# Kernel optimization log

Hardware: AMD Instinct MI355X
Metric: run time of the kernel (lower is better)

The kernel has to match this reference:

```python
import jax, jax.numpy as jnp
import numpy as np

N_STEPS = 8  # fixed-step RK4 over t in [0, 1]


def setup_inputs() -> dict:
    key = jax.random.key(0)
    ks = jax.random.split(key, 5)
    B, T, F, C = 64, 4096, 76, 15
    x = jax.random.normal(ks[0], (B, T, F), dtype=jnp.float32)
    # Conv1d(76->76, k=3) weights, PyTorch OIH layout, fan-in scaled
    conv_w = jax.random.normal(ks[1], (F, F, 3), dtype=jnp.float32) * (1.0 / np.sqrt(F * 3))
    conv_b = jax.random.normal(ks[2], (F,), dtype=jnp.float32) * 0.01
    final_w = jax.random.normal(ks[3], (C, F), dtype=jnp.float32) * (1.0 / np.sqrt(F))
    final_b = jax.random.normal(ks[4], (C,), dtype=jnp.float32) * 0.01
    return {"x": x, "conv_w": conv_w, "conv_b": conv_b,
            "final_w": final_w, "final_b": final_b}


def _func(h, conv_w, conv_b):
    # h: [B, F, T]; Conv1d k=3 pad=1 -> Tanh (the ODE vector field)
    y = jax.lax.conv_general_dilated(
        h, conv_w, window_strides=(1,), padding=[(1, 1)],
        dimension_numbers=("NCH", "OIH", "NCH"))
    return jnp.tanh(y + conv_b[None, :, None])


def reference(x, conv_w, conv_b, final_w, final_b):
    # x: [B, T, F] -> permute to channels-first for Conv1d
    h0 = jnp.transpose(x, (0, 2, 1))  # [B, F, T]
    dt = jnp.float32(1.0 / N_STEPS)

    def rk4_step(h, _):
        k1 = _func(h, conv_w, conv_b)
        k2 = _func(h + 0.5 * dt * k1, conv_w, conv_b)
        k3 = _func(h + 0.5 * dt * k2, conv_w, conv_b)
        k4 = _func(h + dt * k3, conv_w, conv_b)
        return h + (dt / 6.0) * (k1 + 2.0 * k2 + 2.0 * k3 + k4), None

    hT, _ = jax.lax.scan(rk4_step, h0, None, length=N_STEPS)
    # back to [B, T, F], then final Linear(F -> num_classes)
    out = jnp.einsum("bft,cf->btc", hT, final_w) + final_b
    return out
```

## Files before the change

kernel.cpp:

```cpp
#include <hip/hip_runtime.h>
#include <cstdint>
#include <cstddef>

#define F_CH 76
#define T_LEN 4096
#define B_TOT 64
#define C_CLS 15
#define NSTEP 8

#define W_OUT  144
#define HALO2  8
#define NBT    29
#define NKB    5
#define WSTR   88
#define SST    128
#define SROWS  162
#define TPB    960
#define HP     80

#define C2LOG2E 2.8853900817779268f

typedef __attribute__((ext_vector_type(8)))  __bf16 bf16x8;
typedef __attribute__((ext_vector_type(4)))  __bf16 bf16x4;
typedef __attribute__((ext_vector_type(16))) float  f32x16;
typedef __attribute__((ext_vector_type(4)))  float  f32x4;

__device__ __forceinline__ int sw_off(int r, int v) {
    return r * SST + (((v) ^ (r & 15)) << 3);
}

__global__ __launch_bounds__(256) void pad_copy_kernel(
    const float* __restrict__ x, __bf16* __restrict__ h, int b0)
{
    int bl = blockIdx.y;
    int q  = blockIdx.x * 256 + threadIdx.x;
    int t  = q / 20, c4 = (q - t * 20) * 4;
    float4 v = {0.f, 0.f, 0.f, 0.f};
    if (c4 < F_CH)
        v = *(const float4*)(x + ((size_t)(b0 + bl) * T_LEN + t) * F_CH + c4);
    bf16x4 p;
    p[0] = (__bf16)v.x; p[1] = (__bf16)v.y; p[2] = (__bf16)v.z; p[3] = (__bf16)v.w;
    *(bf16x4*)(h + ((size_t)bl * T_LEN + t) * HP + c4) = p;
}

__global__ __launch_bounds__(256) void wprep_kernel(
    const float* __restrict__ cw, __bf16* __restrict__ wpb)
{
    int idx = blockIdx.x * 256 + threadIdx.x;
    if (idx >= 3 * 96 * WSTR) return;
    int tap = idx / (96 * WSTR);
    int rem = idx - tap * 96 * WSTR;
    int c = rem / WSTR, ci = rem - c * WSTR;
    float v = 0.0f;
    if (c < F_CH && ci < F_CH) v = cw[((size_t)c * F_CH + ci) * 3 + tap];
    wpb[idx] = (__bf16)v;
}

__global__ __launch_bounds__(TPB, 4) void rk4_step2_kernel(
    const __bf16* __restrict__ hin, __bf16* __restrict__ hout,
    const __bf16* __restrict__ wpb, const float* __restrict__ cb)
{
    __shared__ __bf16 s_lds[2][SROWS * SST];
    __shared__ float  cb_lds[96];

    const int b    = blockIdx.y;
    const int T0   = blockIdx.x * W_OUT;
    const int tid  = threadIdx.x;
    const int lane = tid & 63;
    const int l31  = lane & 31;
    const int l5   = lane >> 5;
    const int wv   = tid >> 6;
    const int ct   = wv / 5;
    const int tq   = wv - ct * 5;

    const int  rb  = tq * 32 + l31;
    const int  tg  = T0 - HALO2 + rb;
    const bool tok = (tg >= 0 && tg < T_LEN);

    if (tid < 256) {
        int bi = tid / 128, rr = (tid % 128) / 64, c = tid % 64;
        ((uint32_t*)&s_lds[bi][(rr ? (SROWS - 1) : 0) * SST])[c] = 0u;
    }
    if (tid < 96) cb_lds[tid] = (tid < F_CH) ? cb[tid] * C2LOG2E : 0.0f;

    float  hn[16];
    bf16x4 hpk[4];
    const __bf16* hb = hin + (size_t)b * T_LEN * HP;
    #pragma unroll
    for (int q = 0; q < 4; ++q) {
        int c0 = ct * 32 + l5 * 4 + q * 8;
        bf16x4 v = {};
        if (tok && c0 < HP) v = *(const bf16x4*)(hb + (size_t)tg * HP + c0);
        hpk[q] = v;
        hn[q*4+0] = (float)v[0]; hn[q*4+1] = (float)v[1];
        hn[q*4+2] = (float)v[2]; hn[q*4+3] = (float)v[3];
    }

    bf16x8 afr[3][NKB];
    #pragma unroll
    for (int tap = 0; tap < 3; ++tap)
        #pragma unroll
        for (int kb = 0; kb < NKB; ++kb)
            afr[tap][kb] = *(const bf16x8*)&wpb[((size_t)tap * 96 + ct * 32 + l31) * WSTR
                                                + kb * 16 + l5 * 8];

    const float dt = 0.125f;

    #pragma unroll 1
    for (int st = 0; st < 2; ++st) {
        #pragma unroll
        for (int q = 0; q < 4; ++q) {
            int c0 = ct * 32 + l5 * 4 + q * 8;
            if (c0 < HP)
                *(bf16x4*)&s_lds[0][sw_off(rb + 1, ct * 4 + q) + l5 * 4] = hpk[q];
        }
        __syncthreads();

        #pragma unroll 1
        for (int e = 0; e < 4; ++e) {
            const float we   = (e == 0 || e == 3) ? dt / 6.0f : dt / 3.0f;
            const float al   = (e == 2) ? dt : 0.5f * dt;
            const float al_t = tok ? al : 0.0f;

            const __bf16* sb = s_lds[e & 1];
            f32x16 a0 = {};
            #pragma unroll
            for (int tap = 0; tap < 3; ++tap) {
                #pragma unroll
                for (int kb = 0; kb < NKB; ++kb) {
                    bf16x8 bf = *(const bf16x8*)&sb[sw_off(rb + tap, kb * 2 + l5)];
                    a0 = __builtin_amdgcn_mfma_f32_32x32x16_bf16(afr[tap][kb], bf, a0, 0, 0, 0);
                }
            }

            __bf16* sw = s_lds[(e + 1) & 1];
            #pragma unroll
            for (int q = 0; q < 4; ++q) {
                int c0 = ct * 32 + l5 * 4 + q * 8;
                if (c0 >= HP) continue;
                f32x4 bias = *(const f32x4*)&cb_lds[c0];
                bf16x4 p;
                #pragma unroll
                for (int j = 0; j < 4; ++j) {
                    float y  = fmaf(a0[q*4+j], C2LOG2E, bias[j]);
                    float ex = __builtin_amdgcn_exp2f(y);
                    float kv = fmaf(-2.0f, __builtin_amdgcn_rcpf(ex + 1.0f), 1.0f);
                    hn[q*4+j] = fmaf(we, kv, hn[q*4+j]);
                    if (e < 3) p[j] = (__bf16)fmaf(al_t, kv, (float)hpk[q][j]);
                }
                if (e < 3)
                    *(bf16x4*)&sw[sw_off(rb + 1, ct * 4 + q) + l5 * 4] = p;
            }
            if (e < 3) __syncthreads();
        }

        if (st == 0) {
            #pragma unroll
            for (int i = 0; i < 16; ++i) hn[i] = tok ? hn[i] : 0.0f;
            #pragma unroll
            for (int q = 0; q < 4; ++q)
                #pragma unroll
                for (int j = 0; j < 4; ++j) hpk[q][j] = (__bf16)hn[q*4+j];
            __syncthreads();
        }
    }

    if (rb >= HALO2 && rb < HALO2 + W_OUT && tg < T_LEN) {
        __bf16* ho = hout + ((size_t)b * T_LEN + tg) * HP;
        #pragma unroll
        for (int q = 0; q < 4; ++q) {
            int c0 = ct * 32 + l5 * 4 + q * 8;
            if (c0 < HP) {
                bf16x4 p;
                p[0] = (__bf16)hn[q*4+0]; p[1] = (__bf16)hn[q*4+1];
                p[2] = (__bf16)hn[q*4+2]; p[3] = (__bf16)hn[q*4+3];
                *(bf16x4*)(ho + c0) = p;
            }
        }
    }
}

__global__ __launch_bounds__(256) void final_kernel(
    const __bf16* __restrict__ h, const float* __restrict__ fw,
    const float* __restrict__ fb, float* __restrict__ out, int b0)
{
    int bl = blockIdx.y;
    int t  = blockIdx.x * 256 + threadIdx.x;
    const __bf16* hr = h + ((size_t)bl * T_LEN + t) * HP;
    float acc[C_CLS];
#pragma unroll
    for (int c = 0; c < C_CLS; ++c) acc[c] = fb[c];
#pragma unroll
    for (int qf = 0; qf < 19; ++qf) {
        bf16x4 v4 = *(const bf16x4*)(hr + qf * 4);
        float v0 = (float)v4[0], v1 = (float)v4[1], v2 = (float)v4[2], v3 = (float)v4[3];
#pragma unroll
        for (int c = 0; c < C_CLS; ++c) {
            const float* w = fw + c * F_CH + qf * 4;
            acc[c] = fmaf(w[0], v0, acc[c]);
            acc[c] = fmaf(w[1], v1, acc[c]);
            acc[c] = fmaf(w[2], v2, acc[c]);
            acc[c] = fmaf(w[3], v3, acc[c]);
        }
    }
    float* ob = out + ((size_t)(b0 + bl) * T_LEN + t) * C_CLS;
#pragma unroll
    for (int c = 0; c < C_CLS; ++c) ob[c] = acc[c];
}

extern "C" void kernel_launch(void* const* d_in, const int* in_sizes, int n_in,
                              void* d_out, int out_size, void* d_ws, size_t ws_size,
                              hipStream_t stream)
{
    const float* x  = (const float*)d_in[0];
    const float* cw = (const float*)d_in[1];
    const float* cb = (const float*)d_in[2];
    const float* fw = (const float*)d_in[3];
    const float* fb = (const float*)d_in[4];
    float* out = (float*)d_out;

    const size_t FT = (size_t)T_LEN * HP;

    __bf16* WPB = (__bf16*)d_ws;
    const size_t wpbBytes = 51200;
    __bf16* planes = (__bf16*)((char*)d_ws + wpbBytes);

    size_t planeBytes = 2 * FT * sizeof(__bf16);
    size_t avail = ws_size - wpbBytes;
    int Bc = (int)(avail / planeBytes);
    if (Bc > B_TOT) Bc = B_TOT;
    if (Bc < 1) Bc = 1;

    __bf16* H0 = planes;
    __bf16* H1 = H0 + (size_t)Bc * FT;

    wprep_kernel<<<(3 * 96 * WSTR + 255) / 256, 256, 0, stream>>>(cw, WPB);

    for (int b0 = 0; b0 < B_TOT; b0 += Bc) {
        int bc = (B_TOT - b0 < Bc) ? (B_TOT - b0) : Bc;

        dim3 gP(T_LEN * 20 / 256, bc);
        pad_copy_kernel<<<gP, 256, 0, stream>>>(x, H0, b0);

        __bf16* hcur = H0;
        __bf16* hnxt = H1;
        dim3 gR(NBT, bc);
        for (int st2 = 0; st2 < NSTEP / 2; ++st2) {
            rk4_step2_kernel<<<gR, TPB, 0, stream>>>(hcur, hnxt, WPB, cb);
            __bf16* tmp = hcur; hcur = hnxt; hnxt = tmp;
        }

        dim3 gF(T_LEN / 256, bc);
        final_kernel<<<gF, 256, 0, stream>>>(hcur, fw, fb, out, b0);
    }
}
```

Measured before the change: 891.0 us.

## Interleave two time slabs per block to overlap MFMA conv with tanh epilogue

Each block now processes two 112-wide time slabs (A and B) with 768 threads and a triple-buffered LDS ring. The conv MFMAs of one slab are issued while the tanh/RK4 epilogue of the other runs, so matrix and vector work can overlap and barrier stalls are hidden. The third tap's weight fragments are reloaded from global/L2 inside each conv to cut register pressure. In exchange it adds more LDS per block and extra weight loads per stage, and the halo fraction rises because each slab is narrower.

```diff
diff --git a/kernel.cpp b/kernel.cpp
--- a/kernel.cpp
+++ b/kernel.cpp
@@ -8,14 +8,15 @@
 #define C_CLS 15
 #define NSTEP 8
 
-#define W_OUT  144
+#define SLABW  112
+#define BLKW   224
 #define HALO2  8
-#define NBT    29
+#define NBT    19
 #define NKB    5
 #define WSTR   88
 #define SST    128
-#define SROWS  162
-#define TPB    960
+#define SROWS  130
+#define TPB    768
 #define HP     80
 
 #define C2LOG2E 2.8853900817779268f
@@ -56,125 +57,186 @@
     wpb[idx] = (__bf16)v;
 }
 
-__global__ __launch_bounds__(TPB, 4) void rk4_step2_kernel(
+__device__ __forceinline__ f32x16 conv_eval(
+    const __bf16* __restrict__ sb, const __bf16* __restrict__ w2base,
+    int rb, int l5, const bf16x8 afr[2][NKB])
+{
+    bf16x8 a2[NKB];
+    #pragma unroll
+    for (int kb = 0; kb < NKB; ++kb)
+        a2[kb] = *(const bf16x8*)(w2base + kb * 16);
+
+    f32x16 a = {};
+    #pragma unroll
+    for (int tap = 0; tap < 2; ++tap) {
+        #pragma unroll
+        for (int kb = 0; kb < NKB; ++kb) {
+            bf16x8 bf = *(const bf16x8*)&sb[sw_off(rb + tap, kb * 2 + l5)];
+            a = __builtin_amdgcn_mfma_f32_32x32x16_bf16(afr[tap][kb], bf, a, 0, 0, 0);
+        }
+    }
+    #pragma unroll
+    for (int kb = 0; kb < NKB; ++kb) {
+        bf16x8 bf = *(const bf16x8*)&sb[sw_off(rb + 2, kb * 2 + l5)];
+        a = __builtin_amdgcn_mfma_f32_32x32x16_bf16(a2[kb], bf, a, 0, 0, 0);
+    }
+    return a;
+}
+
+__global__ __launch_bounds__(TPB, 3) void rk4_step2_kernel(
     const __bf16* __restrict__ hin, __bf16* __restrict__ hout,
     const __bf16* __restrict__ wpb, const float* __restrict__ cb)
 {
-    __shared__ __bf16 s_lds[2][SROWS * SST];
+    __shared__ __bf16 s_lds[3][SROWS * SST];
     __shared__ float  cb_lds[96];
 
     const int b    = blockIdx.y;
-    const int T0   = blockIdx.x * W_OUT;
+    const int T0A  = blockIdx.x * BLKW;
+    const int T0B  = T0A + SLABW;
     const int tid  = threadIdx.x;
     const int lane = tid & 63;
     const int l31  = lane & 31;
     const int l5   = lane >> 5;
     const int wv   = tid >> 6;
-    const int ct   = wv / 5;
-    const int tq   = wv - ct * 5;
-
-    const int  rb  = tq * 32 + l31;
-    const int  tg  = T0 - HALO2 + rb;
-    const bool tok = (tg >= 0 && tg < T_LEN);
-
-    if (tid < 256) {
-        int bi = tid / 128, rr = (tid % 128) / 64, c = tid % 64;
-        ((uint32_t*)&s_lds[bi][(rr ? (SROWS - 1) : 0) * SST])[c] = 0u;
+    const int ct   = wv >> 2;
+    const int tq   = wv & 3;
+
+    const int  rb   = tq * 32 + l31;
+    const int  tgA  = T0A - HALO2 + rb;
+    const int  tgB  = T0B - HALO2 + rb;
+    const bool tokA = (tgA >= 0 && tgA < T_LEN);
+    const bool tokB = (tgB >= 0 && tgB < T_LEN);
+
+    if (tid < 384) {
+        int buf = tid / 128, rr = (tid % 128) / 64, c = tid % 64;
+        ((uint32_t*)&s_lds[buf][(rr ? (SROWS - 1) : 0) * SST])[c] = 0u;
     }
     if (tid < 96) cb_lds[tid] = (tid < F_CH) ? cb[tid] * C2LOG2E : 0.0f;
 
-    float  hn[16];
-    bf16x4 hpk[4];
+    float  hnA[16], hnB[16];
+    bf16x4 hpkA[4], hpkB[4];
     const __bf16* hb = hin + (size_t)b * T_LEN * HP;
     #pragma unroll
     for (int q = 0; q < 4; ++q) {
         int c0 = ct * 32 + l5 * 4 + q * 8;
-        bf16x4 v = {};
-        if (tok && c0 < HP) v = *(const bf16x4*)(hb + (size_t)tg * HP + c0);
-        hpk[q] = v;
-        hn[q*4+0] = (float)v[0]; hn[q*4+1] = (float)v[1];
-        hn[q*4+2] = (float)v[2]; hn[q*4+3] = (float)v[3];
-    }
-
-    bf16x8 afr[3][NKB];
-    #pragma unroll
-    for (int tap = 0; tap < 3; ++tap)
+        bf16x4 vA = {}, vB = {};
+        if (c0 < HP) {
+            if (tokA) vA = *(const bf16x4*)(hb + (size_t)tgA * HP + c0);
+            if (tokB) vB = *(const bf16x4*)(hb + (size_t)tgB * HP + c0);
+        }
+        hpkA[q] = vA; hpkB[q] = vB;
+        hnA[q*4+0] = (float)vA[0]; hnA[q*4+1] = (float)vA[1];
+        hnA[q*4+2] = (float)vA[2]; hnA[q*4+3] = (float)vA[3];
+        hnB[q*4+0] = (float)vB[0]; hnB[q*4+1] = (float)vB[1];
+        hnB[q*4+2] = (float)vB[2]; hnB[q*4+3] = (float)vB[3];
+    }
+
+    bf16x8 afr[2][NKB];
+    #pragma unroll
+    for (int tap = 0; tap < 2; ++tap)
         #pragma unroll
         for (int kb = 0; kb < NKB; ++kb)
             afr[tap][kb] = *(const bf16x8*)&wpb[((size_t)tap * 96 + ct * 32 + l31) * WSTR
                                                 + kb * 16 + l5 * 8];
+    const __bf16* w2base = wpb + ((size_t)2 * 96 + ct * 32 + l31) * WSTR + l5 * 8;
+
+    __bf16* p0 = s_lds[0];
+    __bf16* p1 = s_lds[1];
+    __bf16* p2 = s_lds[2];
+
+    #pragma unroll
+    for (int q = 0; q < 4; ++q) {
+        int c0 = ct * 32 + l5 * 4 + q * 8;
+        if (c0 < HP) *(bf16x4*)&p0[sw_off(rb + 1, ct * 4 + q) + l5 * 4] = hpkA[q];
+    }
+    __syncthreads();
+
+    f32x16 accA = conv_eval(p0, w2base, rb, l5, afr);
+    #pragma unroll
+    for (int q = 0; q < 4; ++q) {
+        int c0 = ct * 32 + l5 * 4 + q * 8;
+        if (c0 < HP) *(bf16x4*)&p2[sw_off(rb + 1, ct * 4 + q) + l5 * 4] = hpkB[q];
+    }
+    __syncthreads();
 
     const float dt = 0.125f;
+    f32x16 accB;
+
+#define EPI(acc, hn, hpk, tokX, swp)                                          \
+    {                                                                         \
+        const float al_t = (tokX) ? al : 0.0f;                                \
+        _Pragma("unroll")                                                     \
+        for (int q = 0; q < 4; ++q) {                                         \
+            int c0 = ct * 32 + l5 * 4 + q * 8;                                \
+            if (c0 >= HP) continue;                                           \
+            f32x4 bias = *(const f32x4*)&cb_lds[c0];                          \
+            bf16x4 p;                                                         \
+            _Pragma("unroll")                                                 \
+            for (int j = 0; j < 4; ++j) {                                     \
+                float y  = fmaf((acc)[q*4+j], C2LOG2E, bias[j]);              \
+                float ex = __builtin_amdgcn_exp2f(y);                         \
+                float kv = fmaf(-2.0f, __builtin_amdgcn_rcpf(ex + 1.0f), 1.0f); \
+                (hn)[q*4+j] = fmaf(we, kv, (hn)[q*4+j]);                      \
+                p[j] = (__bf16)fmaf(al_t, kv, (float)(hpk)[q][j]);            \
+            }                                                                 \
+            if (!laststage)                                                   \
+                *(bf16x4*)&(swp)[sw_off(rb + 1, ct * 4 + q) + l5 * 4] = p;    \
+        }                                                                     \
+        if (restage) {                                                        \
+            _Pragma("unroll")                                                 \
+            for (int i = 0; i < 16; ++i) (hn)[i] = (tokX) ? (hn)[i] : 0.0f;   \
+            _Pragma("unroll")                                                 \
+            for (int q = 0; q < 4; ++q) {                                     \
+                int c0 = ct * 32 + l5 * 4 + q * 8;                            \
+                _Pragma("unroll")                                             \
+                for (int j = 0; j < 4; ++j) (hpk)[q][j] = (__bf16)(hn)[q*4+j];\
+                if (c0 < HP)                                                  \
+                    *(bf16x4*)&(swp)[sw_off(rb + 1, ct * 4 + q) + l5 * 4] = (hpk)[q]; \
+            }                                                                 \
+        }                                                                     \
+    }
 
     #pragma unroll 1
-    for (int st = 0; st < 2; ++st) {
-        #pragma unroll
-        for (int q = 0; q < 4; ++q) {
-            int c0 = ct * 32 + l5 * 4 + q * 8;
-            if (c0 < HP)
-                *(bf16x4*)&s_lds[0][sw_off(rb + 1, ct * 4 + q) + l5 * 4] = hpk[q];
-        }
+    for (int ge = 0; ge < 8; ++ge) {
+        const float we = (((ge & 3) == 0) || ((ge & 3) == 3)) ? dt / 6.0f : dt / 3.0f;
+        const float al = ((ge & 3) == 2) ? dt : 0.5f * dt;
+        const bool laststage = ((ge & 3) == 3);
+        const bool restage   = (ge == 3);
+
+        accB = conv_eval(p2, w2base, rb, l5, afr);
+        EPI(accA, hnA, hpkA, tokA, p1);
         __syncthreads();
 
-        #pragma unroll 1
-        for (int e = 0; e < 4; ++e) {
-            const float we   = (e == 0 || e == 3) ? dt / 6.0f : dt / 3.0f;
-            const float al   = (e == 2) ? dt : 0.5f * dt;
-            const float al_t = tok ? al : 0.0f;
-
-            const __bf16* sb = s_lds[e & 1];
-            f32x16 a0 = {};
-            #pragma unroll
-            for (int tap = 0; tap < 3; ++tap) {
-                #pragma unroll
-                for (int kb = 0; kb < NKB; ++kb) {
-                    bf16x8 bf = *(const bf16x8*)&sb[sw_off(rb + tap, kb * 2 + l5)];
-                    a0 = __builtin_amdgcn_mfma_f32_32x32x16_bf16(afr[tap][kb], bf, a0, 0, 0, 0);
-                }
-            }
-
-            __bf16* sw = s_lds[(e + 1) & 1];
-            #pragma unroll
-            for (int q = 0; q < 4; ++q) {
-                int c0 = ct * 32 + l5 * 4 + q * 8;
-                if (c0 >= HP) continue;
-                f32x4 bias = *(const f32x4*)&cb_lds[c0];
-                bf16x4 p;
-                #pragma unroll
-                for (int j = 0; j < 4; ++j) {
-                    float y  = fmaf(a0[q*4+j], C2LOG2E, bias[j]);
-                    float ex = __builtin_amdgcn_exp2f(y);
-                    float kv = fmaf(-2.0f, __builtin_amdgcn_rcpf(ex + 1.0f), 1.0f);
-                    hn[q*4+j] = fmaf(we, kv, hn[q*4+j]);
-                    if (e < 3) p[j] = (__bf16)fmaf(al_t, kv, (float)hpk[q][j]);
-                }
-                if (e < 3)
-                    *(bf16x4*)&sw[sw_off(rb + 1, ct * 4 + q) + l5 * 4] = p;
-            }
-            if (e < 3) __syncthreads();
-        }
-
-        if (st == 0) {
-            #pragma unroll
-            for (int i = 0; i < 16; ++i) hn[i] = tok ? hn[i] : 0.0f;
-            #pragma unroll
-            for (int q = 0; q < 4; ++q)
-                #pragma unroll
-                for (int j = 0; j < 4; ++j) hpk[q][j] = (__bf16)hn[q*4+j];
-            __syncthreads();
-        }
-    }
-
-    if (rb >= HALO2 && rb < HALO2 + W_OUT && tg < T_LEN) {
-        __bf16* ho = hout + ((size_t)b * T_LEN + tg) * HP;
+        if (ge < 7) accA = conv_eval(p1, w2base, rb, l5, afr);
+        EPI(accB, hnB, hpkB, tokB, p0);
+        if (ge < 7) __syncthreads();
+
+        __bf16* t = p0; p0 = p1; p1 = p2; p2 = t;
+    }
+#undef EPI
+
+    __bf16* ho = hout + (size_t)b * T_LEN * HP;
+    if (rb >= HALO2 && rb < HALO2 + SLABW && tgA < T_LEN) {
         #pragma unroll
         for (int q = 0; q < 4; ++q) {
             int c0 = ct * 32 + l5 * 4 + q * 8;
             if (c0 < HP) {
                 bf16x4 p;
-                p[0] = (__bf16)hn[q*4+0]; p[1] = (__bf16)hn[q*4+1];
-                p[2] = (__bf16)hn[q*4+2]; p[3] = (__bf16)hn[q*4+3];
-                *(bf16x4*)(ho + c0) = p;
+                p[0] = (__bf16)hnA[q*4+0]; p[1] = (__bf16)hnA[q*4+1];
+                p[2] = (__bf16)hnA[q*4+2]; p[3] = (__bf16)hnA[q*4+3];
+                *(bf16x4*)(ho + (size_t)tgA * HP + c0) = p;
+            }
+        }
+    }
+    if (rb >= HALO2 && rb < HALO2 + SLABW && tgB < T_LEN) {
+        #pragma unroll
+        for (int q = 0; q < 4; ++q) {
+            int c0 = ct * 32 + l5 * 4 + q * 8;
+            if (c0 < HP) {
+                bf16x4 p;
+                p[0] = (__bf16)hnB[q*4+0]; p[1] = (__bf16)hnB[q*4+1];
+                p[2] = (__bf16)hnB[q*4+2]; p[3] = (__bf16)hnB[q*4+3];
+                *(bf16x4*)(ho + (size_t)tgB * HP + c0) = p;
             }
         }
     }
```

After: 2.401 ms. 169% more time.
